# Kernel optimization log

Hardware: AMD Instinct MI355X
Metric: run time of the kernel (lower is better)

The kernel has to match this reference:

```python
import jax, jax.numpy as jnp
import numpy as np

K = 3        # kernel_size
PAD = 1      # padding
STRIDE = 1   # stride


def conv2d(x, w, stride, pad):
    return jax.lax.conv_general_dilated(
        x, w, (stride, stride), [(pad, pad), (pad, pad)],
        dimension_numbers=('NCHW', 'OIHW', 'NCHW'))


def setup_inputs() -> dict:
    key = jax.random.key(0)
    ks = jax.random.split(key, 6)
    B, C, H, W, O = 8, 64, 64, 64, 128
    N = K * K
    x = jax.random.normal(ks[0], (B, C, H, W), jnp.float32)
    # offset (shift) conv: 2N output channels; small weights so sampled
    # positions deviate a few pixels from the regular grid
    shift_w = jax.random.normal(ks[1], (2 * N, C, 3, 3), jnp.float32) * 0.01
    shift_b = jax.random.normal(ks[2], (2 * N,), jnp.float32) * 0.5
    # modulation conv: N output channels
    mod_w = jax.random.normal(ks[3], (N, C, 3, 3), jnp.float32) * 0.01
    mod_b = jax.random.normal(ks[4], (N,), jnp.float32) * 0.1
    # final conv (bias=False), applied with stride=K on the unfolded map
    conv_w = jax.random.normal(ks[5], (O, C, K, K), jnp.float32) / np.sqrt(C * K * K)
    return {'x': x, 'shift_w': shift_w, 'shift_b': shift_b,
            'mod_w': mod_w, 'mod_b': mod_b, 'conv_w': conv_w}


def reference(x, shift_w, shift_b, mod_w, mod_b, conv_w):
    B, C, H, W = x.shape
    k = conv_w.shape[-1]
    N = k * k
    # offsets and modulation from 3x3 convs on the raw input
    offset = conv2d(x, shift_w, STRIDE, 1) + shift_b[None, :, None, None]   # (B,2N,H,W)
    modulation = jax.nn.sigmoid(conv2d(x, mod_w, STRIDE, 1) + mod_b[None, :, None, None])  # (B,N,H,W)

    xp = jnp.pad(x, ((0, 0), (0, 0), (PAD, PAD), (PAD, PAD)))  # zero padding
    Hp, Wp = xp.shape[2], xp.shape[3]

    # p_n: kernel-relative offsets, ij meshgrid, x-block then y-block -> (2N,)
    r = (k - 1) // 2
    pn_x, pn_y = jnp.meshgrid(jnp.arange(-r, r + 1), jnp.arange(-r, r + 1), indexing='ij')
    pn = jnp.concatenate([pn_x.ravel(), pn_y.ravel()]).astype(x.dtype)
    # p_0: base grid starts at 1 (accounts for padding)
    p0x = jnp.broadcast_to(jnp.arange(1, H * STRIDE + 1, STRIDE, dtype=x.dtype)[:, None], (H, W))
    p0y = jnp.broadcast_to(jnp.arange(1, W * STRIDE + 1, STRIDE, dtype=x.dtype)[None, :], (H, W))
    p0 = jnp.concatenate([jnp.broadcast_to(p0x, (N, H, W)),
                          jnp.broadcast_to(p0y, (N, H, W))], 0)  # (2N,H,W)

    pos = offset + pn[None, :, None, None] + p0[None]            # (B,2N,H,W)
    pos = jnp.transpose(pos, (0, 2, 3, 1))                       # (B,H,W,2N)
    px, py = pos[..., :N], pos[..., N:]

    # NOTE: original clamps to output H/W (not padded dims) -- kept faithfully
    fx, fy = jnp.floor(px), jnp.floor(py)
    lt_x = jnp.clip(fx, 0, H - 1).astype(jnp.int32)
    lt_y = jnp.clip(fy, 0, W - 1).astype(jnp.int32)
    rb_x = jnp.clip(fx + 1, 0, H - 1).astype(jnp.int32)
    rb_y = jnp.clip(fy + 1, 0, W - 1).astype(jnp.int32)
    # original casts clamped position to long -> integer bilinear weights
    p_x = jnp.clip(px, 0, H - 1).astype(jnp.int32)
    p_y = jnp.clip(py, 0, W - 1).astype(jnp.int32)

    g_lt = ((1 + (lt_x - p_x)) * (1 + (lt_y - p_y))).astype(x.dtype)
    g_rb = ((1 - (rb_x - p_x)) * (1 - (rb_y - p_y))).astype(x.dtype)
    g_lb = ((1 + (lt_x - p_x)) * (1 + (rb_y - p_y))).astype(x.dtype)  # lb=(lt_x,rb_y)
    g_rt = ((1 - (rb_x - p_x)) * (1 - (lt_y - p_y))).astype(x.dtype)  # rt=(rb_x,lt_y)

    x_flat = xp.reshape(B, C, Hp * Wp)

    def gather(qx, qy):
        idx = (qx * Wp + qy).reshape(B, 1, -1)                     # (B,1,H*W*N)
        v = jnp.take_along_axis(x_flat, jnp.broadcast_to(idx, (B, C, idx.shape[-1])), axis=-1)
        return v.reshape(B, C, H, W, N)

    x_off = (g_lt[:, None] * gather(lt_x, lt_y)
             + g_rb[:, None] * gather(rb_x, rb_y)
             + g_lb[:, None] * gather(lt_x, rb_y)
             + g_rt[:, None] * gather(rb_x, lt_y))                 # (B,C,H,W,N)

    mod = jnp.transpose(modulation, (0, 2, 3, 1))[:, None]        # (B,1,H,W,N)
    x_off = x_off * mod

    # unfold: out[h*k+a, w*k+b] = x_off[h, w, a*k+b]
    x_off = x_off.reshape(B, C, H, W, k, k).transpose(0, 1, 2, 4, 3, 5).reshape(B, C, H * k, W * k)
    return conv2d(x_off, conv_w, k, 0)                            # (B,O,H,W)
```

## Files before the change

### kernel.cpp

```cpp
#include <hip/hip_runtime.h>
#include <hip/hip_fp16.h>
#include <math.h>


typedef _Float16 half8_t __attribute__((ext_vector_type(8)));
typedef float f32x4 __attribute__((ext_vector_type(4)));

__global__ __launch_bounds__(256) void k_pre(const float* __restrict__ x,
                                             const float* __restrict__ cw,
                                             const float* __restrict__ shift_w,
                                             const float* __restrict__ mod_w,
                                             __half* __restrict__ xTh,
                                             __half* __restrict__ xTl,
                                             __half* __restrict__ xCb,
                                             __half* __restrict__ WtF,
                                             __half* __restrict__ WtSFh,
                                             __half* __restrict__ WtSFl) {
    __shared__ float tile[64][65];
    int bid = blockIdx.x;
    int t = threadIdx.x;
    if (bid < 512) {
        int b = bid >> 6, pt = bid & 63;
        int lane = t & 63, cq = t >> 6;
        const float* xb = x + ((size_t)b << 18);
#pragma unroll
        for (int r = 0; r < 16; ++r) {
            int c = cq * 16 + r;
            tile[c][lane] = xb[((size_t)c << 12) + pt * 64 + lane];
        }
        __syncthreads();
        int p = t >> 2, qc = t & 3;
        __align__(16) _Float16 hh[16];
        __align__(16) _Float16 ll[16];
        __align__(16) _Float16 cb[16];
#pragma unroll
        for (int k = 0; k < 16; ++k) {
            float v0 = tile[qc * 16 + k][p];
            float v1 = (p < 63) ? tile[qc * 16 + k][p + 1] : 0.f;
            _Float16 h = (_Float16)v0;
            hh[k] = h;
            ll[k] = (_Float16)(v0 - (float)h);
            cb[k] = (_Float16)(v0 + 2.f * v1);
        }
        size_t off = ((size_t)b << 18) + (size_t)(pt * 64 + p) * 64 + qc * 16;
        ((uint4*)(xTh + off))[0] = ((uint4*)hh)[0];
        ((uint4*)(xTh + off))[1] = ((uint4*)hh)[1];
        ((uint4*)(xTl + off))[0] = ((uint4*)ll)[0];
        ((uint4*)(xTl + off))[1] = ((uint4*)ll)[1];
        ((uint4*)(xCb + off))[0] = ((uint4*)cb)[0];
        ((uint4*)(xCb + off))[1] = ((uint4*)cb)[1];
    } else {
        int u = (bid - 512) * 256 + t;
        if (u < 73728) {
            int e = u & 7, l = (u >> 3) & 63, ks = (u >> 9) & 1;
            int g = (u >> 10) & 3, w = (u >> 12) & 1, n = u >> 13;
            int o = w * 64 + g * 16 + (l & 15);
            int c = ks * 32 + (l >> 4) * 8 + e;
            WtF[u] = __float2half_rn(cw[(o * 64 + c) * 9 + n]);
        } else {
            int q = u - 73728;
            if (q < 18432) {
                int e = q & 7, l = (q >> 3) & 63, nf = (q >> 9) & 1;
                int chf = (q >> 10) & 1, tap = q >> 11;
                int ch = nf * 16 + (l & 15);
                int c = chf * 32 + (l >> 4) * 8 + e;
                float wv = 0.f;
                if (ch < 18) wv = shift_w[(ch * 64 + c) * 9 + tap];
                else if (ch < 27) wv = mod_w[((ch - 18) * 64 + c) * 9 + tap];
                _Float16 h = (_Float16)wv;
                _Float16 lo = (_Float16)(wv - (float)h);
                WtSFh[q] = *(__half*)&h;
                WtSFl[q] = *(__half*)&lo;
            }
        }
    }
}

__global__ __launch_bounds__(256, 4) void k_fused(
    const __half* __restrict__ xTh, const __half* __restrict__ xTl,
    const __half* __restrict__ xCb, const __half* __restrict__ WtF,
    const __half* __restrict__ WtSFh, const __half* __restrict__ WtSFl,
    const float* __restrict__ shift_b, const float* __restrict__ mod_b,
    float* __restrict__ out) {
    __shared__ __align__(16) unsigned char arena[26112];
    __shared__ float Cw[2][2][16][36];
    __shared__ uint4 recA[9][32];

    int t = threadIdx.x;
    int l = t & 63;
    int w = t >> 6;
    int l15 = l & 15, lhi = l >> 4;

    int bid = blockIdx.x;
    int bk = (bid & 7) * 128 + (bid >> 3);
    int b = bk >> 7;
    int u = bk & 127;
    int row = u >> 1;
    int hf = u & 1;
    int col0 = hf * 32;

    const __half* xbh = xTh + ((size_t)b << 18);
    const __half* xbl = xTl + ((size_t)b << 18);
    const __half* xbc = xCb + ((size_t)b << 18);

#pragma unroll
    for (int rr = 0; rr < 7; ++rr) {
        int d = rr * 256 + t;
        if (d < 1632) {
            int bufl = d >= 816 ? 1 : 0;
            int dd = d - bufl * 816;
            int s = dd >> 3, cb8 = dd & 7;
            int r = s / 34, j = s - r * 34;
            int grow = row + r - 1;
            int gcol = col0 - 1 + j;
            uint4 v = make_uint4(0u, 0u, 0u, 0u);
            if ((unsigned)grow < 64u && (unsigned)gcol < 64u) {
                const __half* src = (bufl ? xbl : xbh) +
                                    ((size_t)((grow << 6) + gcol) << 6) + (cb8 << 3);
                v = *(const uint4*)src;
            }
            int dst = bufl * 13056 + s * 128 + ((cb8 << 4) ^ ((s & 7) << 4));
            *(uint4*)&arena[dst] = v;
        }
    }
    __syncthreads();

    {
        int wp = w >> 1, wh = w & 1;
        f32x4 accA[2];
        accA[0] = (f32x4){0.f, 0.f, 0.f, 0.f};
        accA[1] = (f32x4){0.f, 0.f, 0.f, 0.f};
#pragma unroll
        for (int tr = 0; tr < 3; ++tr)
#pragma unroll
            for (int tc = 0; tc < 3; ++tc) {
                int tap = tr * 3 + tc;
                int j = wp * 16 + l15 + tc;
                int s = tr * 34 + j;
                int cbyte = (wh << 6) + (lhi << 4);
                int addr = s * 128 + (cbyte ^ ((s & 7) << 4));
                half8_t Ah = *(const half8_t*)&arena[addr];
                half8_t Al = *(const half8_t*)&arena[13056 + addr];
#pragma unroll
                for (int nf = 0; nf < 2; ++nf) {
                    int fo = ((((tap << 1) + wh) << 1) + nf) << 9;
                    half8_t Bh = *(const half8_t*)(WtSFh + fo + (l << 3));
                    half8_t Bl = *(const half8_t*)(WtSFl + fo + (l << 3));
                    accA[nf] = __builtin_amdgcn_mfma_f32_16x16x32_f16(Ah, Bh, accA[nf], 0, 0, 0);
                    accA[nf] = __builtin_amdgcn_mfma_f32_16x16x32_f16(Ah, Bl, accA[nf], 0, 0, 0);
                    accA[nf] = __builtin_amdgcn_mfma_f32_16x16x32_f16(Al, Bh, accA[nf], 0, 0, 0);
                }
            }
#pragma unroll
        for (int nf = 0; nf < 2; ++nf)
#pragma unroll
            for (int v4 = 0; v4 < 4; ++v4)
                Cw[wh][wp][(lhi << 2) + v4][nf * 16 + l15] = accA[nf][v4];
    }
    __syncthreads();

#pragma unroll
    for (int jj0 = 0; jj0 < 2; ++jj0) {
        int rid = jj0 * 256 + t;
        if (rid < 288) {
            int p = rid & 31;
            int n = rid >> 5;
            int wp = p >> 4, pp = p & 15;
            float sx = Cw[0][wp][pp][n] + Cw[1][wp][pp][n];
            float sy = Cw[0][wp][pp][9 + n] + Cw[1][wp][pp][9 + n];
            float sm = Cw[0][wp][pp][18 + n] + Cw[1][wp][pp][18 + n];
            int jc = col0 + p;

            float px = ((sx + shift_b[n]) + (float)(n / 3 - 1)) + (float)(row + 1);
            float py = ((sy + shift_b[9 + n]) + (float)(n % 3 - 1)) + (float)(jc + 1);
            float mod = 1.f / (1.f + expf(-(sm + mod_b[n])));

            float fx = floorf(px), fy = floorf(py);
            int ltx = (int)fminf(fmaxf(fx, 0.f), 63.f);
            int lty = (int)fminf(fmaxf(fy, 0.f), 63.f);
            int rbx = (int)fminf(fmaxf(fx + 1.f, 0.f), 63.f);
            int rby = (int)fminf(fmaxf(fy + 1.f, 0.f), 63.f);
            int pxi = (int)fminf(fmaxf(px, 0.f), 63.f);
            int pyi = (int)fminf(fmaxf(py, 0.f), 63.f);

            int g_lt = (1 + ltx - pxi) * (1 + lty - pyi);
            int g_rb = (1 - rbx + pxi) * (1 - rby + pyi);
            int g_lb = (1 + ltx - pxi) * (1 + rby - pyi);
            int g_rt = (1 - rbx + pxi) * (1 - lty + pyi);

            bool simple = (ltx == pxi) && (lty == pyi) && (rbx == pxi + 1) &&
                          (rby == pyi + 1) && (ltx >= 1) && (lty >= 1);

            int qxa[4] = {ltx, rbx, ltx, rbx};
            int qya[4] = {lty, rby, rby, lty};
            int gga[4] = {g_lt, g_rb, g_lb, g_rt};
            unsigned w0 = 0, w1 = 0;
#pragma unroll
            for (int jq = 0; jq < 4; ++jq) {
                bool valid = (qxa[jq] >= 1) && (qya[jq] >= 1);
                unsigned idx = valid ? (unsigned)((qxa[jq] - 1) * 64 + (qya[jq] - 1)) : 0u;
                unsigned gc = valid ? (unsigned)gga[jq] : 0u;
                if (jq < 2) w0 |= idx << (12 * jq); else w1 |= idx << (12 * (jq - 2));
                w0 |= gc << (24 + 2 * jq);
            }
            if (simple) w1 |= 0x80000000u;
            recA[n][p] = make_uint4(w0, w1, __float_as_uint(mod), 0u);
        }
    }
    __syncthreads();

    int wm = w >> 1, wn = w & 1;
    int mA = t >> 3, cg = t & 7;

    f32x4 acc[4];
#pragma unroll
    for (int g = 0; g < 4; ++g) acc[g] = (f32x4){0.f, 0.f, 0.f, 0.f};

    for (int n = 0; n < 9; ++n) {
        uint4 Bv[2][4];
#pragma unroll
        for (int ks = 0; ks < 2; ++ks)
#pragma unroll
            for (int g = 0; g < 4; ++g) {
                int fo = ((((((n << 1) + wn) << 2) + g) << 1) + ks) << 9;
                Bv[ks][g] = *(const uint4*)(WtF + fo + (l << 3));
            }

        uint4 rc = recA[n][mA];
        float mod = __uint_as_float(rc.z);
        __align__(16) __half2 a2[4];
        if (rc.y >> 31) {
            int idx = (int)(rc.x & 0xFFF);
            uint4 v = *(const uint4*)(xbc + (idx << 6) + (cg << 3));
            __half mh = __float2half_rn(mod);
            __half2 mm(mh, mh);
            const __half2* vv = (const __half2*)&v;
            a2[0] = __hmul2(mm, vv[0]);
            a2[1] = __hmul2(mm, vv[1]);
            a2[2] = __hmul2(mm, vv[2]);
            a2[3] = __hmul2(mm, vv[3]);
        } else {
            a2[0] = __half2(0, 0); a2[1] = __half2(0, 0);
            a2[2] = __half2(0, 0); a2[3] = __half2(0, 0);
#pragma unroll
            for (int jq = 0; jq < 4; ++jq) {
                int id = (int)((jq < 2 ? (rc.x >> (12 * jq))
                                       : (rc.y >> (12 * (jq - 2)))) & 0xFFF);
                float wf = (float)((rc.x >> (24 + 2 * jq)) & 3) * mod;
                __half2 wh2 = __half2(__float2half_rn(wf), __float2half_rn(wf));
                uint4 v = *(const uint4*)(xbh + (id << 6) + (cg << 3));
                const __half2* vv = (const __half2*)&v;
                a2[0] = __hfma2(wh2, vv[0], a2[0]);
                a2[1] = __hfma2(wh2, vv[1], a2[1]);
                a2[2] = __hfma2(wh2, vv[2], a2[2]);
                a2[3] = __hfma2(wh2, vv[3], a2[3]);
            }
        }
        *(uint4*)&arena[((n & 1) << 12) | (mA << 7) | ((cg ^ (mA & 7)) << 4)] =
            *(uint4*)a2;
        __syncthreads();

#pragma unroll
        for (int ks = 0; ks < 2; ++ks) {
            int rowa = wm * 16 + l15;
            int gr = (ks * 4 + lhi) ^ (rowa & 7);
            half8_t Af = *(const half8_t*)&arena[((n & 1) << 12) | (rowa << 7) | (gr << 4)];
#pragma unroll
            for (int g = 0; g < 4; ++g) {
                half8_t Bf = *(half8_t*)&Bv[ks][g];
                acc[g] = __builtin_amdgcn_mfma_f32_16x16x32_f16(Af, Bf, acc[g], 0, 0, 0);
            }
        }
    }

    float* Ep = (float*)(arena + 8192);
    float* ob = out + ((size_t)b << 19);
    int prow = (row << 6) + col0;
#pragma unroll
    for (int r = 0; r < 4; ++r) {
        if (wn == (r >> 1)) {
#pragma unroll
            for (int gg = 0; gg < 2; ++gg) {
                int g = (r & 1) * 2 + gg;
                int o_loc = gg * 16 + l15;
#pragma unroll
                for (int v4 = 0; v4 < 4; ++v4)
                    Ep[o_loc * 33 + wm * 16 + (lhi << 2) + v4] = acc[g][v4];
            }
        }
        __syncthreads();
        {
            int o_loc = t >> 3;
            int mseg = t & 7;
            float4 fa;
            fa.x = Ep[o_loc * 33 + mseg * 4 + 0];
            fa.y = Ep[o_loc * 33 + mseg * 4 + 1];
            fa.z = Ep[o_loc * 33 + mseg * 4 + 2];
            fa.w = Ep[o_loc * 33 + mseg * 4 + 3];
            float* dst = ob + (((size_t)(r * 32 + o_loc)) << 12) + prow + mseg * 4;
            *(float4*)dst = fa;
        }
        __syncthreads();
    }
}

extern "C" void kernel_launch(void* const* d_in, const int* in_sizes, int n_in,
                              void* d_out, int out_size, void* d_ws, size_t ws_size,
                              hipStream_t stream) {
    const float* x = (const float*)d_in[0];
    const float* shift_w = (const float*)d_in[1];
    const float* shift_b = (const float*)d_in[2];
    const float* mod_w = (const float*)d_in[3];
    const float* mod_b = (const float*)d_in[4];
    const float* conv_w = (const float*)d_in[5];
    float* out = (float*)d_out;

    char* ws = (char*)d_ws;
    __half* xTh = (__half*)ws;
    __half* xTl = (__half*)(ws + 4194304);
    __half* xCb = (__half*)(ws + 8388608);
    __half* WtF = (__half*)(ws + 12582912);
    __half* WtSFh = (__half*)(ws + 12730368);
    __half* WtSFl = (__half*)(ws + 12767232);

    k_pre<<<dim3(872), dim3(256), 0, stream>>>(x, conv_w, shift_w, mod_w,
                                               xTh, xTl, xCb, WtF, WtSFh, WtSFl);
    k_fused<<<dim3(1024), dim3(256), 0, stream>>>(xTh, xTl, xCb, WtF, WtSFh,
                                                  WtSFl, shift_b, mod_b, out);
}
```

Baseline: 39.16 us.

## Process full 64-pixel rows per block and stage final-conv weights in LDS

Each fused block now covers a whole output row (64 pixels) with 512 threads instead of half a row with 256, halving the grid and sharing the halo tile and per-tap weights across twice as many pixels. Per-tap final-conv weights are copied cooperatively into a double-buffered LDS slot instead of each wave loading them into registers from global memory. The epilogue writes all 128 output channels in one LDS pass rather than four synchronized rounds. The cost is roughly double the shared memory per block and fewer resident blocks, so occupancy and latency hiding may drop. The grid also shrinks to 512 blocks, which may underfill the GPU.

```diff
diff --git a/kernel.cpp b/kernel.cpp
--- a/kernel.cpp
+++ b/kernel.cpp
@@ -76,15 +76,15 @@
     }
 }
 
-__global__ __launch_bounds__(256, 4) void k_fused(
+__global__ __launch_bounds__(512, 2) void k_fused(
     const __half* __restrict__ xTh, const __half* __restrict__ xTl,
     const __half* __restrict__ xCb, const __half* __restrict__ WtF,
     const __half* __restrict__ WtSFh, const __half* __restrict__ WtSFl,
     const float* __restrict__ shift_b, const float* __restrict__ mod_b,
     float* __restrict__ out) {
-    __shared__ __align__(16) unsigned char arena[26112];
-    __shared__ float Cw[2][2][16][36];
-    __shared__ uint4 recA[9][32];
+    __shared__ __align__(16) unsigned char arena[50688];
+    __shared__ float Cw[2][4][16][36];
+    __shared__ uint4 recA[9][64];
 
     int t = threadIdx.x;
     int l = t & 63;
@@ -92,12 +92,9 @@
     int l15 = l & 15, lhi = l >> 4;
 
     int bid = blockIdx.x;
-    int bk = (bid & 7) * 128 + (bid >> 3);
-    int b = bk >> 7;
-    int u = bk & 127;
-    int row = u >> 1;
-    int hf = u & 1;
-    int col0 = hf * 32;
+    int bk = (bid & 7) * 64 + (bid >> 3);
+    int b = bk >> 6;
+    int row = bk & 63;
 
     const __half* xbh = xTh + ((size_t)b << 18);
     const __half* xbl = xTl + ((size_t)b << 18);
@@ -105,21 +102,21 @@
 
 #pragma unroll
     for (int rr = 0; rr < 7; ++rr) {
-        int d = rr * 256 + t;
-        if (d < 1632) {
-            int bufl = d >= 816 ? 1 : 0;
-            int dd = d - bufl * 816;
+        int d = rr * 512 + t;
+        if (d < 3168) {
+            int bufl = d >= 1584 ? 1 : 0;
+            int dd = d - bufl * 1584;
             int s = dd >> 3, cb8 = dd & 7;
-            int r = s / 34, j = s - r * 34;
+            int r = s / 66, j = s - r * 66;
             int grow = row + r - 1;
-            int gcol = col0 - 1 + j;
+            int gcol = j - 1;
             uint4 v = make_uint4(0u, 0u, 0u, 0u);
             if ((unsigned)grow < 64u && (unsigned)gcol < 64u) {
                 const __half* src = (bufl ? xbl : xbh) +
                                     ((size_t)((grow << 6) + gcol) << 6) + (cb8 << 3);
                 v = *(const uint4*)src;
             }
-            int dst = bufl * 13056 + s * 128 + ((cb8 << 4) ^ ((s & 7) << 4));
+            int dst = bufl * 25344 + s * 128 + ((cb8 << 4) ^ ((s & 7) << 4));
             *(uint4*)&arena[dst] = v;
         }
     }
@@ -136,11 +133,11 @@
             for (int tc = 0; tc < 3; ++tc) {
                 int tap = tr * 3 + tc;
                 int j = wp * 16 + l15 + tc;
-                int s = tr * 34 + j;
+                int s = tr * 66 + j;
                 int cbyte = (wh << 6) + (lhi << 4);
                 int addr = s * 128 + (cbyte ^ ((s & 7) << 4));
                 half8_t Ah = *(const half8_t*)&arena[addr];
-                half8_t Al = *(const half8_t*)&arena[13056 + addr];
+                half8_t Al = *(const half8_t*)&arena[25344 + addr];
 #pragma unroll
                 for (int nf = 0; nf < 2; ++nf) {
                     int fo = ((((tap << 1) + wh) << 1) + nf) << 9;
@@ -161,18 +158,17 @@
 
 #pragma unroll
     for (int jj0 = 0; jj0 < 2; ++jj0) {
-        int rid = jj0 * 256 + t;
-        if (rid < 288) {
-            int p = rid & 31;
-            int n = rid >> 5;
+        int rid = jj0 * 512 + t;
+        if (rid < 576) {
+            int p = rid & 63;
+            int n = rid >> 6;
             int wp = p >> 4, pp = p & 15;
             float sx = Cw[0][wp][pp][n] + Cw[1][wp][pp][n];
             float sy = Cw[0][wp][pp][9 + n] + Cw[1][wp][pp][9 + n];
             float sm = Cw[0][wp][pp][18 + n] + Cw[1][wp][pp][18 + n];
-            int jc = col0 + p;
 
             float px = ((sx + shift_b[n]) + (float)(n / 3 - 1)) + (float)(row + 1);
-            float py = ((sy + shift_b[9 + n]) + (float)(n % 3 - 1)) + (float)(jc + 1);
+            float py = ((sy + shift_b[9 + n]) + (float)(n % 3 - 1)) + (float)(p + 1);
             float mod = 1.f / (1.f + expf(-(sm + mod_b[n])));
 
             float fx = floorf(px), fy = floorf(py);
@@ -217,90 +213,90 @@
     for (int g = 0; g < 4; ++g) acc[g] = (f32x4){0.f, 0.f, 0.f, 0.f};
 
     for (int n = 0; n < 9; ++n) {
-        uint4 Bv[2][4];
-#pragma unroll
-        for (int ks = 0; ks < 2; ++ks)
-#pragma unroll
-            for (int g = 0; g < 4; ++g) {
-                int fo = ((((((n << 1) + wn) << 2) + g) << 1) + ks) << 9;
-                Bv[ks][g] = *(const uint4*)(WtF + fo + (l << 3));
-            }
-
-        uint4 rc = recA[n][mA];
-        float mod = __uint_as_float(rc.z);
-        __align__(16) __half2 a2[4];
-        if (rc.y >> 31) {
-            int idx = (int)(rc.x & 0xFFF);
-            uint4 v = *(const uint4*)(xbc + (idx << 6) + (cg << 3));
-            __half mh = __float2half_rn(mod);
-            __half2 mm(mh, mh);
-            const __half2* vv = (const __half2*)&v;
-            a2[0] = __hmul2(mm, vv[0]);
-            a2[1] = __hmul2(mm, vv[1]);
-            a2[2] = __hmul2(mm, vv[2]);
-            a2[3] = __hmul2(mm, vv[3]);
-        } else {
-            a2[0] = __half2(0, 0); a2[1] = __half2(0, 0);
-            a2[2] = __half2(0, 0); a2[3] = __half2(0, 0);
-#pragma unroll
-            for (int jq = 0; jq < 4; ++jq) {
-                int id = (int)((jq < 2 ? (rc.x >> (12 * jq))
-                                       : (rc.y >> (12 * (jq - 2)))) & 0xFFF);
-                float wf = (float)((rc.x >> (24 + 2 * jq)) & 3) * mod;
-                __half2 wh2 = __half2(__float2half_rn(wf), __float2half_rn(wf));
-                uint4 v = *(const uint4*)(xbh + (id << 6) + (cg << 3));
+        int sl = n & 1;
+        {
+            const uint4* wsrc = (const uint4*)(WtF + n * 8192);
+            uint4* wdst = (uint4*)&arena[16384 + (sl << 14)];
+            wdst[t] = wsrc[t];
+            wdst[512 + t] = wsrc[512 + t];
+        }
+
+        {
+            uint4 rc = recA[n][mA];
+            float mod = __uint_as_float(rc.z);
+            __align__(16) __half2 a2[4];
+            if (rc.y >> 31) {
+                int idx = (int)(rc.x & 0xFFF);
+                uint4 v = *(const uint4*)(xbc + (idx << 6) + (cg << 3));
+                __half mh = __float2half_rn(mod);
+                __half2 mm(mh, mh);
                 const __half2* vv = (const __half2*)&v;
-                a2[0] = __hfma2(wh2, vv[0], a2[0]);
-                a2[1] = __hfma2(wh2, vv[1], a2[1]);
-                a2[2] = __hfma2(wh2, vv[2], a2[2]);
-                a2[3] = __hfma2(wh2, vv[3], a2[3]);
-            }
-        }
-        *(uint4*)&arena[((n & 1) << 12) | (mA << 7) | ((cg ^ (mA & 7)) << 4)] =
-            *(uint4*)a2;
+                a2[0] = __hmul2(mm, vv[0]);
+                a2[1] = __hmul2(mm, vv[1]);
+                a2[2] = __hmul2(mm, vv[2]);
+                a2[3] = __hmul2(mm, vv[3]);
+            } else {
+                a2[0] = __half2(0, 0); a2[1] = __half2(0, 0);
+                a2[2] = __half2(0, 0); a2[3] = __half2(0, 0);
+#pragma unroll
+                for (int jq = 0; jq < 4; ++jq) {
+                    int id = (int)((jq < 2 ? (rc.x >> (12 * jq))
+                                           : (rc.y >> (12 * (jq - 2)))) & 0xFFF);
+                    float wf = (float)((rc.x >> (24 + 2 * jq)) & 3) * mod;
+                    __half2 wh2 = __half2(__float2half_rn(wf), __float2half_rn(wf));
+                    uint4 v = *(const uint4*)(xbh + (id << 6) + (cg << 3));
+                    const __half2* vv = (const __half2*)&v;
+                    a2[0] = __hfma2(wh2, vv[0], a2[0]);
+                    a2[1] = __hfma2(wh2, vv[1], a2[1]);
+                    a2[2] = __hfma2(wh2, vv[2], a2[2]);
+                    a2[3] = __hfma2(wh2, vv[3], a2[3]);
+                }
+            }
+            *(uint4*)&arena[(sl << 13) | (mA << 7) | ((cg ^ (mA & 7)) << 4)] =
+                *(uint4*)a2;
+        }
         __syncthreads();
 
+        const unsigned char* wsl = &arena[16384 + (sl << 14)];
 #pragma unroll
         for (int ks = 0; ks < 2; ++ks) {
             int rowa = wm * 16 + l15;
             int gr = (ks * 4 + lhi) ^ (rowa & 7);
-            half8_t Af = *(const half8_t*)&arena[((n & 1) << 12) | (rowa << 7) | (gr << 4)];
+            half8_t Af = *(const half8_t*)&arena[(sl << 13) | (rowa << 7) | (gr << 4)];
 #pragma unroll
             for (int g = 0; g < 4; ++g) {
-                half8_t Bf = *(half8_t*)&Bv[ks][g];
+                half8_t Bf = *(const half8_t*)&wsl[((((wn << 2) + g) << 1) + ks) * 1024 +
+                                                   (l << 4)];
                 acc[g] = __builtin_amdgcn_mfma_f32_16x16x32_f16(Af, Bf, acc[g], 0, 0, 0);
             }
         }
     }
 
-    float* Ep = (float*)(arena + 8192);
-    float* ob = out + ((size_t)b << 19);
-    int prow = (row << 6) + col0;
-#pragma unroll
-    for (int r = 0; r < 4; ++r) {
-        if (wn == (r >> 1)) {
-#pragma unroll
-            for (int gg = 0; gg < 2; ++gg) {
-                int g = (r & 1) * 2 + gg;
-                int o_loc = gg * 16 + l15;
-#pragma unroll
-                for (int v4 = 0; v4 < 4; ++v4)
-                    Ep[o_loc * 33 + wm * 16 + (lhi << 2) + v4] = acc[g][v4];
-            }
-        }
-        __syncthreads();
-        {
-            int o_loc = t >> 3;
-            int mseg = t & 7;
+    __syncthreads();
+    float* Ep = (float*)arena;
+#pragma unroll
+    for (int g = 0; g < 4; ++g) {
+        int o_loc = (wn << 6) + (g << 4) + l15;
+#pragma unroll
+        for (int v4 = 0; v4 < 4; ++v4)
+            Ep[o_loc * 65 + (wm << 4) + (lhi << 2) + v4] = acc[g][v4];
+    }
+    __syncthreads();
+    {
+        float* ob = out + ((size_t)b << 19);
+        int prow = row << 6;
+#pragma unroll
+        for (int r = 0; r < 4; ++r) {
+            int o_loc = (r << 5) + (t >> 4);
+            int mseg = t & 15;
             float4 fa;
-            fa.x = Ep[o_loc * 33 + mseg * 4 + 0];
-            fa.y = Ep[o_loc * 33 + mseg * 4 + 1];
-            fa.z = Ep[o_loc * 33 + mseg * 4 + 2];
-            fa.w = Ep[o_loc * 33 + mseg * 4 + 3];
-            float* dst = ob + (((size_t)(r * 32 + o_loc)) << 12) + prow + mseg * 4;
+            fa.x = Ep[o_loc * 65 + mseg * 4 + 0];
+            fa.y = Ep[o_loc * 65 + mseg * 4 + 1];
+            fa.z = Ep[o_loc * 65 + mseg * 4 + 2];
+            fa.w = Ep[o_loc * 65 + mseg * 4 + 3];
+            float* dst = ob + (((size_t)o_loc) << 12) + prow + mseg * 4;
             *(float4*)dst = fa;
         }
-        __syncthreads();
     }
 }
 
@@ -325,6 +321,6 @@
 
     k_pre<<<dim3(872), dim3(256), 0, stream>>>(x, conv_w, shift_w, mod_w,
                                                xTh, xTl, xCb, WtF, WtSFh, WtSFl);
-    k_fused<<<dim3(1024), dim3(256), 0, stream>>>(xTh, xTl, xCb, WtF, WtSFh,
-                                                  WtSFl, shift_b, mod_b, out);
+    k_fused<<<dim3(512), dim3(512), 0, stream>>>(xTh, xTl, xCb, WtF, WtSFh,
+                                                 WtSFl, shift_b, mod_b, out);
 }
```

After: 36.45 us. 6.9% less time.
